# Kernel tuning notes

Hardware: AMD Instinct MI355X
Metric: run time of the kernel (lower is better)

Reference implementation:

```python
import jax, jax.numpy as jnp
import numpy as np

# Config matching init_kwargs
PCR = (-51.2, -51.2, -5.0, 51.2, 51.2, 3.0)  # point cloud range
PS = 0.2                                      # pillar size
GW = int(round((PCR[3] - PCR[0]) / PS))       # 512 bev width
GH = int(round((PCR[4] - PCR[1]) / PS))       # 512 bev height
B = 4
N = 800000
CIN = 4
COUT = 32


def setup_inputs() -> dict:
    key = jax.random.key(0)
    k1, k2, k3 = jax.random.split(key, 3)
    u = jax.random.uniform(k1, (N, 3), dtype=jnp.float32)
    # points uniformly inside the point cloud range
    lo = jnp.array([PCR[0], PCR[1], PCR[2]], dtype=jnp.float32)
    ext = jnp.array([PCR[3] - PCR[0], PCR[4] - PCR[1], PCR[5] - PCR[2]], dtype=jnp.float32)
    xyz = u * ext + lo
    xyz_batch_cnt = jnp.full((B,), N // B, dtype=jnp.int32)
    pt_feature = jax.random.normal(k2, (N, CIN), dtype=jnp.float32)
    W = jax.random.normal(k3, (CIN + 3, COUT), dtype=jnp.float32) * 0.1  # xavier-ish shared MLP
    return {"xyz": xyz, "xyz_batch_cnt": xyz_batch_cnt, "pt_feature": pt_feature, "W": W}


def reference(xyz, xyz_batch_cnt, pt_feature, W):
    # point -> batch index (FGPillarQueryAndGroup grouping)
    b_idx = jnp.repeat(jnp.arange(B, dtype=jnp.int32), xyz_batch_cnt, total_repeat_length=N)
    # point -> pillar (x,y) cell
    px = jnp.clip(jnp.floor((xyz[:, 0] - PCR[0]) / PS).astype(jnp.int32), 0, GW - 1)
    py = jnp.clip(jnp.floor((xyz[:, 1] - PCR[1]) / PS).astype(jnp.int32), 0, GH - 1)
    # pillar centers; relative offsets are the grouped geometric features
    cx = (px.astype(xyz.dtype) + 0.5) * PS + PCR[0]
    cy = (py.astype(xyz.dtype) + 0.5) * PS + PCR[1]
    cz = 0.5 * (PCR[2] + PCR[5])
    offs = jnp.stack([xyz[:, 0] - cx, xyz[:, 1] - cy, xyz[:, 2] - cz], axis=1)  # (N,3)
    group_features = jnp.concatenate([pt_feature, offs], axis=1)               # (N, CIN+3)
    # shared MLP (1x1 conv == linear) + ReLU
    h = jax.nn.relu(group_features @ W)                                        # (N, COUT)
    # scatter-max pooling over pillar segments (dense BEV layout: b*H*W + y*W + x)
    seg = b_idx * (GH * GW) + py * GW + px
    pooled = jax.ops.segment_max(h, seg, num_segments=B * GH * GW)             # (B*H*W, COUT)
    pooled = jnp.where(jnp.isfinite(pooled), pooled, jnp.zeros((), pooled.dtype))
    return pooled
```

## Files before the change

### kernel.cpp

```cpp
#include <hip/hip_runtime.h>


#define GW 512
#define GH 512
#define COUT 32
#define PTS_PER_BLOCK 8

__global__ __launch_bounds__(256) void pillar_fwd(
    const float* __restrict__ xyz,
    const int*   __restrict__ cnt,
    const float4* __restrict__ feat,
    const float* __restrict__ W,
    int* __restrict__ out,
    unsigned char* __restrict__ touched,
    int N, int B)
{
    __shared__ float sW[7 * COUT];
    int tid = threadIdx.x;
    if (tid < 7 * COUT) sW[tid] = W[tid];
    __syncthreads();

    int p = blockIdx.x * PTS_PER_BLOCK + (tid >> 5);
    int c = tid & 31;
    if (p >= N) return;

    float x = xyz[3 * p + 0];
    float y = xyz[3 * p + 1];
    float z = xyz[3 * p + 2];

    int b = 0, acc = 0;
    for (int k = 0; k < B; ++k) {
        acc += cnt[k];
        b += (p >= acc) ? 1 : 0;
    }

    int px = (int)floorf((x - (-51.2f)) / 0.2f);
    int py = (int)floorf((y - (-51.2f)) / 0.2f);
    px = min(max(px, 0), GW - 1);
    py = min(max(py, 0), GH - 1);

    float cx = ((float)px + 0.5f) * 0.2f + (-51.2f);
    float cy = ((float)py + 0.5f) * 0.2f + (-51.2f);
    float g4 = x - cx;
    float g5 = y - cy;
    float g6 = z + 1.0f;

    float4 f = feat[p];

    float h = f.x * sW[0 * COUT + c]
            + f.y * sW[1 * COUT + c]
            + f.z * sW[2 * COUT + c]
            + f.w * sW[3 * COUT + c]
            + g4  * sW[4 * COUT + c]
            + g5  * sW[5 * COUT + c]
            + g6  * sW[6 * COUT + c];
    h = fmaxf(h, 0.0f);

    unsigned seg = (unsigned)b * (GH * GW) + (unsigned)py * GW + (unsigned)px;
    if (c == 0) touched[seg] = 1;
    atomicMax(out + (size_t)seg * COUT + c, __float_as_int(h));
}

__global__ __launch_bounds__(256) void fill_empty(
    const unsigned char* __restrict__ touched,
    float4* __restrict__ out, int ncells)
{
    int idx = blockIdx.x * 256 + threadIdx.x;
    int cell = idx >> 3;
    if (cell >= ncells) return;
    if (touched[cell]) return;
    out[(size_t)cell * 8 + (idx & 7)] = make_float4(0.f, 0.f, 0.f, 0.f);
}


__global__ __launch_bounds__(256) void zero_out(uint4* __restrict__ out, int n4)
{
    int stride = gridDim.x * 256;
    for (int i = blockIdx.x * 256 + threadIdx.x; i < n4; i += stride)
        out[i] = make_uint4(0u, 0u, 0u, 0u);
}

__global__ __launch_bounds__(256) void pillar_fwd_zeroed(
    const float* __restrict__ xyz, const int* __restrict__ cnt,
    const float4* __restrict__ feat, const float* __restrict__ W,
    unsigned int* __restrict__ out, int N, int B)
{
    __shared__ float sW[7 * COUT];
    int tid = threadIdx.x;
    if (tid < 7 * COUT) sW[tid] = W[tid];
    __syncthreads();
    int p = blockIdx.x * PTS_PER_BLOCK + (tid >> 5);
    int c = tid & 31;
    if (p >= N) return;
    float x = xyz[3 * p + 0], y = xyz[3 * p + 1], z = xyz[3 * p + 2];
    int b = 0, acc = 0;
    for (int k = 0; k < B; ++k) { acc += cnt[k]; b += (p >= acc) ? 1 : 0; }
    int px = (int)floorf((x - (-51.2f)) / 0.2f);
    int py = (int)floorf((y - (-51.2f)) / 0.2f);
    px = min(max(px, 0), GW - 1);
    py = min(max(py, 0), GH - 1);
    float cx = ((float)px + 0.5f) * 0.2f + (-51.2f);
    float cy = ((float)py + 0.5f) * 0.2f + (-51.2f);
    float4 f = feat[p];
    float h = f.x * sW[0 * COUT + c] + f.y * sW[1 * COUT + c]
            + f.z * sW[2 * COUT + c] + f.w * sW[3 * COUT + c]
            + (x - cx) * sW[4 * COUT + c] + (y - cy) * sW[5 * COUT + c]
            + (z + 1.0f) * sW[6 * COUT + c];
    h = fmaxf(h, 0.0f);
    unsigned seg = (unsigned)b * (GH * GW) + (unsigned)py * GW + (unsigned)px;
    atomicMax(out + (size_t)seg * COUT + c, __float_as_uint(h));
}

extern "C" void kernel_launch(void* const* d_in, const int* in_sizes, int n_in,
                              void* d_out, int out_size, void* d_ws, size_t ws_size,
                              hipStream_t stream) {
    const float*  xyz  = (const float*)d_in[0];
    const int*    cnt  = (const int*)d_in[1];
    const float4* feat = (const float4*)d_in[2];
    const float*  W    = (const float*)d_in[3];

    int N = in_sizes[0] / 3;
    int B = in_sizes[1];
    int ncells = B * GH * GW;

    int grid = (N + PTS_PER_BLOCK - 1) / PTS_PER_BLOCK;

    if (ws_size >= (size_t)ncells) {
        unsigned char* touched = (unsigned char*)d_ws;
        hipMemsetAsync(touched, 0, (size_t)ncells, stream);
        pillar_fwd<<<grid, 256, 0, stream>>>(xyz, cnt, feat, W,
                                             (int*)d_out, touched, N, B);
        int fgrid = (ncells * 8 + 255) / 256;
        fill_empty<<<fgrid, 256, 0, stream>>>(touched, (float4*)d_out, ncells);
    } else {
        int n4 = out_size / 4;
        zero_out<<<2048, 256, 0, stream>>>((uint4*)d_out, n4);
        pillar_fwd_zeroed<<<grid, 256, 0, stream>>>(xyz, cnt, feat, W,
                                                    (unsigned int*)d_out, N, B);
    }
}
```

Baseline: 283.7 us.

## Bucket raw point records into output lines, then compute MLP max per pillar

Replaces the per-channel atomicMax scatter with a two-pass scheme. Each point claims a slot in its pillar's 32-float output line with one atomicAdd and stores its 7 input features there, capped at 4 records per pillar. Points beyond the cap go to an overflow list that a third kernel applies with atomicMax. A pooling pass reads each line, evaluates the shared MLP, and writes the max, which also zero-fills empty cells. This removes 32 atomics per point and the touched-byte pass, at the cost of a 4 MB counts memset, a full-output read pass, and more kernel launches.

```diff
diff --git a/kernel.cpp b/kernel.cpp
--- a/kernel.cpp
+++ b/kernel.cpp
@@ -4,74 +4,118 @@
 #define GW 512
 #define GH 512
 #define COUT 32
-#define PTS_PER_BLOCK 8
+#define CAP 4
+#define RECF 7
 
-__global__ __launch_bounds__(256) void pillar_fwd(
-    const float* __restrict__ xyz,
-    const int*   __restrict__ cnt,
+struct OvRec { unsigned seg; float f0, f1, f2, f3, g4, g5, g6; };
+
+__device__ __forceinline__ int batch_of(int p, const int* __restrict__ cnt, int B) {
+    int b = 0, acc = 0;
+    for (int k = 0; k < B; ++k) { acc += cnt[k]; b += (p >= acc) ? 1 : 0; }
+    return min(b, B - 1);
+}
+
+__device__ __forceinline__ void cell_of(float x, float y, int& px, int& py) {
+    px = (int)floorf((x - (-51.2f)) / 0.2f);
+    py = (int)floorf((y - (-51.2f)) / 0.2f);
+    px = min(max(px, 0), GW - 1);
+    py = min(max(py, 0), GH - 1);
+}
+
+__global__ __launch_bounds__(256) void bucket_scatter(
+    const float* __restrict__ xyz, const int* __restrict__ cnt,
     const float4* __restrict__ feat,
-    const float* __restrict__ W,
-    int* __restrict__ out,
-    unsigned char* __restrict__ touched,
+    unsigned* __restrict__ counts,
+    unsigned* __restrict__ gcount,
+    OvRec* __restrict__ list,
+    unsigned ocap,
+    float* __restrict__ out,
     int N, int B)
 {
-    __shared__ float sW[7 * COUT];
-    int tid = threadIdx.x;
-    if (tid < 7 * COUT) sW[tid] = W[tid];
-    __syncthreads();
-
-    int p = blockIdx.x * PTS_PER_BLOCK + (tid >> 5);
-    int c = tid & 31;
+    int p = blockIdx.x * 256 + threadIdx.x;
     if (p >= N) return;
-
     float x = xyz[3 * p + 0];
     float y = xyz[3 * p + 1];
     float z = xyz[3 * p + 2];
-
-    int b = 0, acc = 0;
-    for (int k = 0; k < B; ++k) {
-        acc += cnt[k];
-        b += (p >= acc) ? 1 : 0;
-    }
-
-    int px = (int)floorf((x - (-51.2f)) / 0.2f);
-    int py = (int)floorf((y - (-51.2f)) / 0.2f);
-    px = min(max(px, 0), GW - 1);
-    py = min(max(py, 0), GH - 1);
-
+    int b = batch_of(p, cnt, B);
+    int px, py; cell_of(x, y, px, py);
     float cx = ((float)px + 0.5f) * 0.2f + (-51.2f);
     float cy = ((float)py + 0.5f) * 0.2f + (-51.2f);
-    float g4 = x - cx;
-    float g5 = y - cy;
-    float g6 = z + 1.0f;
+    float g4 = x - cx, g5 = y - cy, g6 = z + 1.0f;
+    float4 f = feat[p];
+    unsigned seg = (unsigned)b * (GH * GW) + (unsigned)py * GW + (unsigned)px;
 
-    float4 f = feat[p];
-
-    float h = f.x * sW[0 * COUT + c]
-            + f.y * sW[1 * COUT + c]
-            + f.z * sW[2 * COUT + c]
-            + f.w * sW[3 * COUT + c]
-            + g4  * sW[4 * COUT + c]
-            + g5  * sW[5 * COUT + c]
-            + g6  * sW[6 * COUT + c];
-    h = fmaxf(h, 0.0f);
-
-    unsigned seg = (unsigned)b * (GH * GW) + (unsigned)py * GW + (unsigned)px;
-    if (c == 0) touched[seg] = 1;
-    atomicMax(out + (size_t)seg * COUT + c, __float_as_int(h));
+    unsigned slot = atomicAdd(&counts[seg], 1u);
+    if (slot < CAP) {
+        float* dst = out + (size_t)seg * COUT + slot * RECF;
+        dst[0] = f.x; dst[1] = f.y; dst[2] = f.z; dst[3] = f.w;
+        dst[4] = g4;  dst[5] = g5;  dst[6] = g6;
+    } else {
+        unsigned oi = atomicAdd(gcount, 1u);
+        if (oi < ocap) {
+            OvRec r; r.seg = seg;
+            r.f0 = f.x; r.f1 = f.y; r.f2 = f.z; r.f3 = f.w;
+            r.g4 = g4;  r.g5 = g5;  r.g6 = g6;
+            list[oi] = r;
+        }
+    }
 }
 
-__global__ __launch_bounds__(256) void fill_empty(
-    const unsigned char* __restrict__ touched,
-    float4* __restrict__ out, int ncells)
+__global__ __launch_bounds__(256) void pool_lines(
+    const unsigned* __restrict__ counts, const float* __restrict__ W,
+    float* __restrict__ out, int ncells)
 {
-    int idx = blockIdx.x * 256 + threadIdx.x;
-    int cell = idx >> 3;
+    int tid = threadIdx.x;
+    int cell = blockIdx.x * 8 + (tid >> 5);
+    int c = tid & 31;
     if (cell >= ncells) return;
-    if (touched[cell]) return;
-    out[(size_t)cell * 8 + (idx & 7)] = make_float4(0.f, 0.f, 0.f, 0.f);
+
+    float w0 = W[0 * COUT + c], w1 = W[1 * COUT + c], w2 = W[2 * COUT + c];
+    float w3 = W[3 * COUT + c], w4 = W[4 * COUT + c], w5 = W[5 * COUT + c];
+    float w6 = W[6 * COUT + c];
+
+    unsigned m = counts[cell];
+    if (m > CAP) m = CAP;
+    const float* line = out + (size_t)cell * COUT;
+
+    float best = 0.0f;
+    for (unsigned j = 0; j < m; ++j) {
+        float f0 = line[j * RECF + 0], f1 = line[j * RECF + 1];
+        float f2 = line[j * RECF + 2], f3 = line[j * RECF + 3];
+        float g4 = line[j * RECF + 4], g5 = line[j * RECF + 5];
+        float g6 = line[j * RECF + 6];
+        float h = f0 * w0 + f1 * w1 + f2 * w2 + f3 * w3
+                + g4 * w4 + g5 * w5 + g6 * w6;
+        best = fmaxf(best, h);
+    }
+    out[(size_t)cell * COUT + c] = best;
 }
 
+__global__ __launch_bounds__(256) void overflow_fix(
+    const unsigned* __restrict__ gcount, const OvRec* __restrict__ list,
+    const float* __restrict__ W, int* __restrict__ out, unsigned ocap)
+{
+    __shared__ float sW[RECF * COUT];
+    int tid = threadIdx.x;
+    if (tid < RECF * COUT) sW[tid] = W[tid];
+    __syncthreads();
+
+    unsigned total = *gcount;
+    if (total > ocap) total = ocap;
+    int c = tid & 31;
+    unsigned stride = gridDim.x * 8;
+    for (unsigned i = blockIdx.x * 8 + (tid >> 5); i < total; i += stride) {
+        OvRec r = list[i];
+        float h = r.f0 * sW[0 * COUT + c] + r.f1 * sW[1 * COUT + c]
+                + r.f2 * sW[2 * COUT + c] + r.f3 * sW[3 * COUT + c]
+                + r.g4 * sW[4 * COUT + c] + r.g5 * sW[5 * COUT + c]
+                + r.g6 * sW[6 * COUT + c];
+        atomicMax(out + (size_t)r.seg * COUT + c, __float_as_int(h));
+    }
+}
+
+
+#define PTS_PER_BLOCK 8
 
 __global__ __launch_bounds__(256) void zero_out(uint4* __restrict__ out, int n4)
 {
@@ -85,20 +129,16 @@
     const float4* __restrict__ feat, const float* __restrict__ W,
     unsigned int* __restrict__ out, int N, int B)
 {
-    __shared__ float sW[7 * COUT];
+    __shared__ float sW[RECF * COUT];
     int tid = threadIdx.x;
-    if (tid < 7 * COUT) sW[tid] = W[tid];
+    if (tid < RECF * COUT) sW[tid] = W[tid];
     __syncthreads();
     int p = blockIdx.x * PTS_PER_BLOCK + (tid >> 5);
     int c = tid & 31;
     if (p >= N) return;
     float x = xyz[3 * p + 0], y = xyz[3 * p + 1], z = xyz[3 * p + 2];
-    int b = 0, acc = 0;
-    for (int k = 0; k < B; ++k) { acc += cnt[k]; b += (p >= acc) ? 1 : 0; }
-    int px = (int)floorf((x - (-51.2f)) / 0.2f);
-    int py = (int)floorf((y - (-51.2f)) / 0.2f);
-    px = min(max(px, 0), GW - 1);
-    py = min(max(py, 0), GH - 1);
+    int b = batch_of(p, cnt, B);
+    int px, py; cell_of(x, y, px, py);
     float cx = ((float)px + 0.5f) * 0.2f + (-51.2f);
     float cy = ((float)py + 0.5f) * 0.2f + (-51.2f);
     float4 f = feat[p];
@@ -123,18 +163,30 @@
     int B = in_sizes[1];
     int ncells = B * GH * GW;
 
-    int grid = (N + PTS_PER_BLOCK - 1) / PTS_PER_BLOCK;
+    size_t offCounts = 256;
+    size_t offList   = (offCounts + (size_t)ncells * 4 + 255) & ~(size_t)255;
+    size_t needed    = offList + (size_t)N * sizeof(OvRec);
 
-    if (ws_size >= (size_t)ncells) {
-        unsigned char* touched = (unsigned char*)d_ws;
-        hipMemsetAsync(touched, 0, (size_t)ncells, stream);
-        pillar_fwd<<<grid, 256, 0, stream>>>(xyz, cnt, feat, W,
-                                             (int*)d_out, touched, N, B);
-        int fgrid = (ncells * 8 + 255) / 256;
-        fill_empty<<<fgrid, 256, 0, stream>>>(touched, (float4*)d_out, ncells);
+    if (ws_size >= needed) {
+        char* ws = (char*)d_ws;
+        unsigned* gcount = (unsigned*)ws;
+        unsigned* counts = (unsigned*)(ws + offCounts);
+        OvRec*    list   = (OvRec*)(ws + offList);
+        unsigned  ocap   = (unsigned)N;
+
+        hipMemsetAsync(ws, 0, offCounts + (size_t)ncells * 4, stream);
+
+        int gpts = (N + 255) / 256;
+        bucket_scatter<<<gpts, 256, 0, stream>>>(xyz, cnt, feat, counts, gcount,
+                                                 list, ocap, (float*)d_out, N, B);
+        pool_lines<<<(ncells + 7) / 8, 256, 0, stream>>>(counts, W,
+                                                         (float*)d_out, ncells);
+        overflow_fix<<<256, 256, 0, stream>>>(gcount, list, W,
+                                              (int*)d_out, ocap);
     } else {
         int n4 = out_size / 4;
         zero_out<<<2048, 256, 0, stream>>>((uint4*)d_out, n4);
+        int grid = (N + PTS_PER_BLOCK - 1) / PTS_PER_BLOCK;
         pillar_fwd_zeroed<<<grid, 256, 0, stream>>>(xyz, cnt, feat, W,
                                                     (unsigned int*)d_out, N, B);
     }
```

Measured after the change: 319.1 us. 12.5% more time.
